# Performance work log

Hardware: AMD Instinct MI355X
Metric: run time of the kernel (lower is better)

## Reference

```python
import jax, jax.numpy as jnp
import numpy as np

NUM_HEADS = 16
LAMBDA = 0.1
HADAMARD_SCALE = 0.05
ROPE_BASE = 10000.0


def _rope(t):
    # t: [B, H, S, hd] -- rotary embedding (half-split convention)
    hd = t.shape[-1]
    S = t.shape[2]
    half = hd // 2
    inv_freq = 1.0 / (ROPE_BASE ** (jnp.arange(half, dtype=jnp.float32) / half))
    ang = jnp.arange(S, dtype=jnp.float32)[:, None] * inv_freq[None, :]  # [S, half]
    cos = jnp.cos(ang).astype(t.dtype)
    sin = jnp.sin(ang).astype(t.dtype)
    t1, t2 = t[..., :half], t[..., half:]
    return jnp.concatenate([t1 * cos - t2 * sin, t2 * cos + t1 * sin], axis=-1)


def _rotate_half(t):
    half = t.shape[-1] // 2
    return jnp.concatenate([-t[..., half:], t[..., :half]], axis=-1)


def setup_inputs() -> dict:
    key = jax.random.key(0)
    ks = jax.random.split(key, 6)
    B, S, D = 2, 2048, 1024
    scale = 1.0 / np.sqrt(D).astype(np.float32)
    x = jax.random.normal(ks[0], (B, S, D), jnp.float32)
    Wq = jax.random.normal(ks[1], (D, D), jnp.float32) * scale
    Wk = jax.random.normal(ks[2], (D, D), jnp.float32) * scale
    Wv = jax.random.normal(ks[3], (D, D), jnp.float32) * scale
    Wo = jax.random.normal(ks[4], (D, D), jnp.float32) * scale
    gate_w = jax.random.normal(ks[5], (D // NUM_HEADS,), jnp.float32) * 0.01
    return {"x": x, "Wq": Wq, "Wk": Wk, "Wv": Wv, "Wo": Wo, "gate_w": gate_w}


def reference(x, Wq, Wk, Wv, Wo, gate_w):
    B, S, D = x.shape
    H = NUM_HEADS
    hd = D // H

    def heads(W):
        return (x @ W.T).reshape(B, S, H, hd).transpose(0, 2, 1, 3)  # [B,H,S,hd]

    Q = _rope(heads(Wq))
    K = _rope(heads(Wk))
    V = heads(Wv)

    causal = jnp.tril(jnp.ones((S, S), dtype=bool))
    inv_sqrt_d = 1.0 / jnp.sqrt(jnp.asarray(hd, x.dtype))

    def attend(q, k):
        # first-order + lambda * second-order (elementwise-squared) scores
        s = (jnp.einsum('bhsd,bhtd->bhst', q, k)
             + LAMBDA * jnp.einsum('bhsd,bhtd->bhst', q * q, k * k)) * inv_sqrt_d
        s = jnp.where(causal, s, jnp.asarray(-1e9, s.dtype))
        a = jax.nn.softmax(s, axis=-1)
        return jnp.einsum('bhst,bhtd->bhsd', a, V)

    out1 = attend(Q, K)                                  # standard pass
    out2 = attend(_rotate_half(Q), _rotate_half(K))      # rotated second pass

    # hadamard gate mix of the two passes
    out = 0.5 * (out1 + out2) + HADAMARD_SCALE * (out1 * out2) * gate_w

    out = out.transpose(0, 2, 1, 3).reshape(B, S, D)
    return out @ Wo.T
```

## Files before the change

kernel.cpp:

```cpp
#include <hip/hip_runtime.h>

typedef unsigned short u16;
typedef __attribute__((ext_vector_type(4))) unsigned short u16x4;
typedef __attribute__((ext_vector_type(8))) unsigned short u16x8;
typedef __attribute__((ext_vector_type(8))) short s16x8;
typedef __attribute__((ext_vector_type(4))) float f32x4;

__device__ __forceinline__ u16 f2bf(float f) {
  unsigned int u = __float_as_uint(f);
  u += 0x7FFFu + ((u >> 16) & 1u);
  return (u16)(u >> 16);
}
__device__ __forceinline__ float bf2f(u16 h) {
  return __uint_as_float(((unsigned int)h) << 16);
}

__device__ __forceinline__ void gload_lds16(const u16* g, u16* l) {
  __builtin_amdgcn_global_load_lds(
      (const __attribute__((address_space(1))) unsigned int*)(g),
      (__attribute__((address_space(3))) unsigned int*)(l), 16, 0, 0);
}

__global__ __launch_bounds__(256) void cvt_all(const float* __restrict__ x,
                                               const float* __restrict__ Wq,
                                               const float* __restrict__ Wk,
                                               const float* __restrict__ Wv,
                                               const float* __restrict__ Wo,
                                               u16* __restrict__ xbf,
                                               u16* __restrict__ wbf,
                                               u16* __restrict__ wobf) {
  int blk = blockIdx.x;
  const float* src;
  u16* dst;
  int i;
  if (blk < 4096) {
    src = x; dst = xbf; i = blk * 256 + threadIdx.x;
  } else {
    int wb = blk - 4096;
    int sel = wb >> 10;
    src = (sel == 0) ? Wq : (sel == 1) ? Wk : (sel == 2) ? Wv : Wo;
    dst = (sel < 3) ? (wbf + (size_t)sel * 1048576) : wobf;
    i = (wb & 1023) * 256 + threadIdx.x;
  }
  float4 v = reinterpret_cast<const float4*>(src)[i];
  u16x4 o;
  o.x = f2bf(v.x); o.y = f2bf(v.y); o.z = f2bf(v.z); o.w = f2bf(v.w);
  reinterpret_cast<u16x4*>(dst)[i] = o;
}

__device__ __forceinline__ void store_out(float* p, float v) { *p = v; }
__device__ __forceinline__ void store_out(u16* p, float v) { *p = f2bf(v); }

template <typename OutT, int WM, int WN>
__global__ __launch_bounds__(256) void gemm_bt(const u16* __restrict__ A,
                                               const u16* __restrict__ Bw,
                                               OutT* __restrict__ C, int N, int K) {
  __shared__ u16 As[2][WM * 1024];
  __shared__ u16 Bs[2][WN * 1024];
  const int tid = threadIdx.x;
  const int lane = tid & 63;
  const int wave = tid >> 6;
  const int wm = wave >> 1, wn = wave & 1;
  const int lh = lane & 15, quad = lane >> 4;
  const int q8 = quad * 8;
  const int m0 = blockIdx.y * (WM * 32), n0 = blockIdx.x * (WN * 32);
  constexpr int NCH = 2 * (WM + WN);
  constexpr int PER = NCH / 4;

  auto stage = [&](int buf, int kt) {
    const int kb = kt * 32;
#pragma unroll
    for (int i = 0; i < PER; ++i) {
      const int c = wave * PER + i;
      if (c < 2 * WM) {
        gload_lds16(A + (size_t)(m0 + c * 16 + lh) * K + kb + q8,
                    &As[buf][c * 512 + lane * 8]);
      } else {
        const int rb = c - 2 * WM;
        gload_lds16(Bw + (size_t)(n0 + rb * 16 + lh) * K + kb + q8,
                    &Bs[buf][rb * 512 + lane * 8]);
      }
    }
  };

  f32x4 acc[WM][WN];
#pragma unroll
  for (int i = 0; i < WM; ++i)
#pragma unroll
    for (int j = 0; j < WN; ++j) { acc[i][j][0] = 0.f; acc[i][j][1] = 0.f; acc[i][j][2] = 0.f; acc[i][j][3] = 0.f; }

  const int nkt = K >> 5;
  stage(0, 0);
  __syncthreads();
  for (int kt = 0; kt < nkt; ++kt) {
    const int p = kt & 1;
    if (kt < nkt - 1) stage(1 - p, kt + 1);
    s16x8 af[WM], bf4[WN];
#pragma unroll
    for (int mb = 0; mb < WM; ++mb)
      af[mb] = *reinterpret_cast<const s16x8*>(&As[p][(wm * WM + mb) * 512 + lane * 8]);
#pragma unroll
    for (int nb = 0; nb < WN; ++nb)
      bf4[nb] = *reinterpret_cast<const s16x8*>(&Bs[p][(wn * WN + nb) * 512 + lane * 8]);
#pragma unroll
    for (int mb = 0; mb < WM; ++mb)
#pragma unroll
      for (int nb = 0; nb < WN; ++nb)
        acc[mb][nb] = __builtin_amdgcn_mfma_f32_16x16x32_bf16(af[mb], bf4[nb], acc[mb][nb], 0, 0, 0);
    __syncthreads();
  }
#pragma unroll
  for (int mb = 0; mb < WM; ++mb)
#pragma unroll
    for (int nb = 0; nb < WN; ++nb) {
      const int col = n0 + wn * (WN * 16) + nb * 16 + lh;
#pragma unroll
      for (int r = 0; r < 4; ++r) {
        const int row = m0 + wm * (WM * 16) + mb * 16 + quad * 4 + r;
        store_out(&C[(size_t)row * N + col], acc[mb][nb][r]);
      }
    }
}

__global__ __launch_bounds__(256) void qkv_gemm(const u16* __restrict__ A,
                                                const u16* __restrict__ Bw,
                                                u16* __restrict__ Vt,
                                                u16* __restrict__ Qs,
                                                u16* __restrict__ Kb,
                                                u16* __restrict__ K2b) {
  __shared__ u16 As[2][4096];
  __shared__ u16 Bs[2][4096];
  const int tid = threadIdx.x;
  const int lane = tid & 63;
  const int wave = tid >> 6;
  const int wm = wave >> 1, wn = wave & 1;
  const int lh = lane & 15, quad = lane >> 4;
  const int q8 = quad * 8;
  const int bx = blockIdx.x;
  const int m0 = blockIdx.y * 128, n0 = bx * 128;
  const int K = 1024;

  auto stage = [&](int buf, int kt) {
    const int kb = kt * 32;
#pragma unroll
    for (int i = 0; i < 4; ++i) {
      const int c = wave * 4 + i;
      if (c < 8) {
        gload_lds16(A + (size_t)(m0 + c * 16 + lh) * K + kb + q8,
                    &As[buf][c * 512 + lane * 8]);
      } else {
        const int rb = c - 8;
        gload_lds16(Bw + (size_t)(n0 + rb * 16 + lh) * K + kb + q8,
                    &Bs[buf][rb * 512 + lane * 8]);
      }
    }
  };

  f32x4 acc[4][4];
#pragma unroll
  for (int i = 0; i < 4; ++i)
#pragma unroll
    for (int j = 0; j < 4; ++j) { acc[i][j][0] = 0.f; acc[i][j][1] = 0.f; acc[i][j][2] = 0.f; acc[i][j][3] = 0.f; }

  stage(0, 0);
  __syncthreads();
  for (int kt = 0; kt < 32; ++kt) {
    const int p = kt & 1;
    if (kt < 31) stage(1 - p, kt + 1);
    s16x8 af[4], bf4[4];
#pragma unroll
    for (int mb = 0; mb < 4; ++mb)
      af[mb] = *reinterpret_cast<const s16x8*>(&As[p][(wm * 4 + mb) * 512 + lane * 8]);
#pragma unroll
    for (int nb = 0; nb < 4; ++nb)
      bf4[nb] = *reinterpret_cast<const s16x8*>(&Bs[p][(wn * 4 + nb) * 512 + lane * 8]);
#pragma unroll
    for (int mb = 0; mb < 4; ++mb)
#pragma unroll
      for (int nb = 0; nb < 4; ++nb)
        acc[mb][nb] = __builtin_amdgcn_mfma_f32_16x16x32_bf16(af[mb], bf4[nb], acc[mb][nb], 0, 0, 0);
    __syncthreads();
  }

  if (bx < 16) {
    const bool isQ = (bx < 8);
#pragma unroll
    for (int nb = 0; nb < 2; ++nb) {
      const int d = nb * 16 + lh;
      const float invf = __expf((float)d * -0.2878231366f);
      const int col = n0 + wn * 64 + nb * 16 + lh;
      const int ch = col & 1023;
      const int h = ch >> 6;
#pragma unroll
      for (int mb = 0; mb < 4; ++mb)
#pragma unroll
        for (int r = 0; r < 4; ++r) {
          const int row = m0 + wm * 64 + mb * 16 + quad * 4 + r;
          const int s = row & 2047, b = row >> 11;
          float ang = (float)s * invf;
          float sv, cv;
          __sincosf(ang, &sv, &cv);
          const float v1 = acc[mb][nb][r], v2 = acc[mb][nb + 2][r];
          const float e0 = v1 * cv - v2 * sv;
          const float e1 = v2 * cv + v1 * sv;
          const size_t ofs = (size_t)((b * 16 + h) * 2048 + s) * 64 + d;
          if (isQ) {
            Qs[ofs]      = f2bf(e0 * 0.125f);
            Qs[ofs + 32] = f2bf(e1 * 0.125f);
          } else {
            Kb[ofs]       = f2bf(e0);
            Kb[ofs + 32]  = f2bf(e1);
            K2b[ofs]      = f2bf(e0 * e0);
            K2b[ofs + 32] = f2bf(e1 * e1);
          }
        }
    }
  } else {
#pragma unroll
    for (int mb = 0; mb < 4; ++mb)
#pragma unroll
      for (int nb = 0; nb < 4; ++nb) {
        const int col = n0 + wn * 64 + nb * 16 + lh;
        const int ch = col & 1023;
        const int h = ch >> 6, d = ch & 63;
        const int row0 = m0 + wm * 64 + mb * 16 + quad * 4;
        const int s0 = row0 & 2047, b = row0 >> 11;
        u16x4 o;
#pragma unroll
        for (int r = 0; r < 4; ++r) o[r] = f2bf(acc[mb][nb][r]);
        *reinterpret_cast<u16x4*>(Vt + (size_t)((b * 16 + h) * 64 + d) * 2048 + s0) = o;
      }
  }
}

__global__ __launch_bounds__(256, 2) void attn_kernel(const u16* __restrict__ Qs,
                                                      const u16* __restrict__ Kb,
                                                      const u16* __restrict__ K2b,
                                                      const u16* __restrict__ Vt,
                                                      const float* __restrict__ gate,
                                                      u16* __restrict__ attn,
                                                      float* __restrict__ Opart,
                                                      float* __restrict__ Lpart,
                                                      float* __restrict__ Opart2,
                                                      float* __restrict__ Lpart2) {
  const int bx = blockIdx.x;
  int qi, kt0, kt1, chunk, which;
  bool split;
  if (bx < 32) {
    qi = 15 - (bx >> 2); chunk = bx & 3; split = true; which = 0;
    const int T = 2 * qi + 2;
    kt0 = (chunk * T) >> 2;
    kt1 = (((chunk + 1) * T) >> 2) - 1;
  } else if (bx < 40) {
    const int t = bx - 32;
    qi = 7 - (t >> 1); chunk = t & 1; split = true; which = 1;
    const int nk = qi + 1; kt0 = chunk * nk; kt1 = kt0 + nk - 1;
  } else {
    qi = 43 - bx; split = false; which = 0; chunk = 0; kt0 = 0; kt1 = 2 * qi + 1;
  }
  const int bh = blockIdx.y;
  const int tid = threadIdx.x, lane = tid & 63, wave = tid >> 6;
  const int lh = lane & 15, quad = lane >> 4;
  const int b = bh >> 4, h = bh & 15;
  __shared__ u16 stageS[2][8192];
  __shared__ u16 Pbuf[4][2][1152];
  const int base = qi * 128 + wave * 32;
  const int q8 = quad * 8;

  auto do_stage = [&](int buf, int kt) {
#pragma unroll
    for (int i = 0; i < 4; ++i) {
      const int c = wave * 4 + i;
      const int t2 = c >> 3, f = c & 7, kk = f >> 2, nb = f & 3;
      const u16* src = (t2 ? K2b : Kb) +
          (size_t)(bh * 2048 + kt * 64 + nb * 16 + lh) * 64 + kk * 32 + q8;
      gload_lds16(src, &stageS[buf][t2 * 4096 + f * 512 + lane * 8]);
    }
  };

  s16x8 qf[2][2], q2f[2][2];
#pragma unroll
  for (int mb = 0; mb < 2; ++mb) {
    const size_t qoff = (size_t)(bh * 2048 + base + mb * 16 + lh) * 64 + q8;
#pragma unroll
    for (int kk = 0; kk < 2; ++kk) {
      qf[mb][kk] = *reinterpret_cast<const s16x8*>(Qs + qoff + kk * 32);
#pragma unroll
      for (int j = 0; j < 8; ++j) {
        float f = bf2f((u16)qf[mb][kk][j]);
        q2f[mb][kk][j] = (short)f2bf(f * f * 0.8f);
      }
    }
  }

  f32x4 oacc[2][4];
  float lsum[2][4];
#pragma unroll
  for (int mb = 0; mb < 2; ++mb)
#pragma unroll
    for (int nb = 0; nb < 4; ++nb) { oacc[mb][nb][0] = 0.f; oacc[mb][nb][1] = 0.f; oacc[mb][nb][2] = 0.f; oacc[mb][nb][3] = 0.f; }
#pragma unroll
  for (int mb = 0; mb < 2; ++mb)
#pragma unroll
    for (int r = 0; r < 4; ++r) lsum[mb][r] = 0.f;
  float gw[4];
#pragma unroll
  for (int nb = 0; nb < 4; ++nb) gw[nb] = gate[nb * 16 + lh];

  do_stage(0, kt0);
  __syncthreads();

  const int wmaxrow = base + 31;
  for (int kt = kt0; kt <= kt1; ++kt) {
    const int p = (kt - kt0) & 1;
    if (kt < kt1) do_stage(1 - p, kt + 1);

    if (kt * 64 <= wmaxrow) {
      const u16* Ks = stageS[p];
      f32x4 sacc[2][4];
#pragma unroll
      for (int mb = 0; mb < 2; ++mb)
#pragma unroll
        for (int nb = 0; nb < 4; ++nb) { sacc[mb][nb][0] = -8.f; sacc[mb][nb][1] = -8.f; sacc[mb][nb][2] = -8.f; sacc[mb][nb][3] = -8.f; }
#pragma unroll
      for (int nb = 0; nb < 4; ++nb)
#pragma unroll
        for (int kk = 0; kk < 2; ++kk) {
          s16x8 kf  = *reinterpret_cast<const s16x8*>(&Ks[(kk * 4 + nb) * 512 + lane * 8]);
          s16x8 k2f = *reinterpret_cast<const s16x8*>(&Ks[4096 + (kk * 4 + nb) * 512 + lane * 8]);
#pragma unroll
          for (int mb = 0; mb < 2; ++mb) {
            sacc[mb][nb] = __builtin_amdgcn_mfma_f32_16x16x32_bf16(qf[mb][kk],  kf,  sacc[mb][nb], 0, 0, 0);
            sacc[mb][nb] = __builtin_amdgcn_mfma_f32_16x16x32_bf16(q2f[mb][kk], k2f, sacc[mb][nb], 0, 0, 0);
          }
        }
      s16x8 vf[2][4];
#pragma unroll
      for (int kk = 0; kk < 2; ++kk)
#pragma unroll
        for (int nb = 0; nb < 4; ++nb)
          vf[kk][nb] = *reinterpret_cast<const s16x8*>(
              Vt + (size_t)(bh * 64 + nb * 16 + lh) * 2048 + kt * 64 + kk * 32 + q8);

      if (kt * 64 + 63 > base) {
#pragma unroll
        for (int mb = 0; mb < 2; ++mb)
#pragma unroll
          for (int nb = 0; nb < 4; ++nb) {
            const int colg = kt * 64 + nb * 16 + lh;
#pragma unroll
            for (int r = 0; r < 4; ++r) {
              const int rowg = base + mb * 16 + quad * 4 + r;
              if (colg > rowg) sacc[mb][nb][r] = -1e9f;
            }
          }
      }
#pragma unroll
      for (int mb = 0; mb < 2; ++mb)
#pragma unroll
        for (int nb = 0; nb < 4; ++nb)
#pragma unroll
          for (int r = 0; r < 4; ++r) {
            float pv = __expf(sacc[mb][nb][r]);
            lsum[mb][r] += pv;
            Pbuf[wave][mb][(quad * 4 + r) * 72 + nb * 16 + lh] = f2bf(pv);
          }
#pragma unroll
      for (int mb = 0; mb < 2; ++mb)
#pragma unroll
        for (int kk = 0; kk < 2; ++kk) {
          s16x8 pf = *reinterpret_cast<const s16x8*>(&Pbuf[wave][mb][lh * 72 + kk * 32 + q8]);
#pragma unroll
          for (int nb = 0; nb < 4; ++nb)
            oacc[mb][nb] = __builtin_amdgcn_mfma_f32_16x16x32_bf16(pf, vf[kk][nb], oacc[mb][nb], 0, 0, 0);
        }
    }
    __syncthreads();
  }
#pragma unroll
  for (int mb = 0; mb < 2; ++mb)
#pragma unroll
    for (int r = 0; r < 4; ++r) {
      float rs = lsum[mb][r];
#pragma unroll
      for (int off = 1; off < 16; off <<= 1) rs += __shfl_xor(rs, off);
      lsum[mb][r] = rs;
    }
  if (split) {
#pragma unroll
    for (int mb = 0; mb < 2; ++mb)
#pragma unroll
      for (int r = 0; r < 4; ++r) {
        const int rowg = base + mb * 16 + quad * 4 + r;
        if (which == 0) {
          const size_t orow = (size_t)chunk * 32768 + bh * 1024 + (rowg - 1024);
          if (lh == 0) Lpart[orow] = lsum[mb][r];
#pragma unroll
          for (int nb = 0; nb < 4; ++nb)
            Opart[orow * 64 + nb * 16 + lh] = oacc[mb][nb][r];
        } else {
          const size_t orow = (size_t)chunk * 16384 + bh * 512 + (rowg - 512);
          if (lh == 0) Lpart2[orow] = lsum[mb][r];
#pragma unroll
          for (int nb = 0; nb < 4; ++nb)
            Opart2[orow * 64 + nb * 16 + lh] = oacc[mb][nb][r];
        }
      }
  } else {
#pragma unroll
    for (int mb = 0; mb < 2; ++mb)
#pragma unroll
      for (int r = 0; r < 4; ++r) {
        const float invl = 1.0f / lsum[mb][r];
        const int rows = base + mb * 16 + quad * 4 + r;
#pragma unroll
        for (int nb = 0; nb < 4; ++nb) {
          float o = oacc[mb][nb][r] * invl;
          float val = o + 0.05f * o * o * gw[nb];
          attn[(size_t)(b * 2048 + rows) * 1024 + h * 64 + nb * 16 + lh] = f2bf(val);
        }
      }
  }
}

__global__ __launch_bounds__(256) void combine_kernel(const float* __restrict__ Opart,
                                                      const float* __restrict__ Lpart,
                                                      const float* __restrict__ Opart2,
                                                      const float* __restrict__ Lpart2,
                                                      const float* __restrict__ gate,
                                                      u16* __restrict__ attn) {
  int idx = blockIdx.x * 256 + threadIdx.x;
  int d = idx & 63;
  int r_all = idx >> 6;
  float o, l;
  int bh, s;
  if (r_all < 32768) {
    o = Opart[idx] + Opart[idx + 2097152] + Opart[idx + 4194304] + Opart[idx + 6291456];
    l = Lpart[r_all] + Lpart[r_all + 32768] + Lpart[r_all + 65536] + Lpart[r_all + 98304];
    bh = r_all >> 10; s = 1024 + (r_all & 1023);
  } else {
    const int r2 = r_all - 32768;
    const int i2 = idx - 2097152;
    o = Opart2[i2] + Opart2[i2 + 1048576];
    l = Lpart2[r2] + Lpart2[r2 + 16384];
    bh = r2 >> 9; s = 512 + (r2 & 511);
  }
  o /= l;
  float val = o + 0.05f * o * o * gate[d];
  int b = bh >> 4, h = bh & 15;
  attn[(size_t)(b * 2048 + s) * 1024 + h * 64 + d] = f2bf(val);
}

extern "C" void kernel_launch(void* const* d_in, const int* in_sizes, int n_in,
                              void* d_out, int out_size, void* d_ws, size_t ws_size,
                              hipStream_t stream) {
  (void)in_sizes; (void)n_in; (void)out_size; (void)ws_size;
  const float* x    = (const float*)d_in[0];
  const float* Wq   = (const float*)d_in[1];
  const float* Wk   = (const float*)d_in[2];
  const float* Wv   = (const float*)d_in[3];
  const float* Wo   = (const float*)d_in[4];
  const float* gate = (const float*)d_in[5];

  u16* ws    = (u16*)d_ws;
  u16* xbf   = ws;
  u16* wbf   = xbf + 4194304;
  u16* wobf  = wbf + 3145728;
  u16* Qsb   = wobf + 1048576;
  u16* Kbb   = Qsb + 4194304;
  u16* K2bb  = Kbb + 4194304;
  u16* Vtb   = K2bb + 4194304;
  float* Opart  = (float*)(Vtb + 4194304);
  float* Lpart  = Opart + 8388608;
  float* Opart2 = Lpart + 131072;
  float* Lpart2 = Opart2 + 2097152;
  u16* attnb = xbf;

  cvt_all<<<8192, 256, 0, stream>>>(x, Wq, Wk, Wv, Wo, xbf, wbf, wobf);
  qkv_gemm<<<dim3(24, 32), 256, 0, stream>>>(xbf, wbf, Vtb, Qsb, Kbb, K2bb);
  attn_kernel<<<dim3(44, 32), 256, 0, stream>>>(Qsb, Kbb, K2bb, Vtb, gate, attnb,
                                                Opart, Lpart, Opart2, Lpart2);
  combine_kernel<<<12288, 256, 0, stream>>>(Opart, Lpart, Opart2, Lpart2, gate, attnb);
  gemm_bt<float, 4, 2><<<dim3(16, 32), 256, 0, stream>>>(attnb, wobf, (float*)d_out, 1024, 1024);
}
```

Baseline: 244.0 us.

## Drop LDS K staging, load K directly, remap blocks per XCD, raise occupancy

Removes the double-buffered shared-memory staging of K and K² tiles and the per-iteration __syncthreads, so each wave reads its K fragments straight from global memory. Each wave stops its loop at its own diagonal tile instead of idling inside a block-wide barrier. Blocks are remapped so the 44 query chunks of a head land on the same XCD for L2 reuse, and launch bounds go from 2 to 4 blocks per CU. s_setprio hints are added around the MFMA sections. The cost is redundant global/L2 traffic for K across the four waves and more register pressure under the higher occupancy bound.

```diff
diff --git a/kernel.cpp b/kernel.cpp
--- a/kernel.cpp
+++ b/kernel.cpp
@@ -233,7 +233,7 @@
   }
 }
 
-__global__ __launch_bounds__(256, 2) void attn_kernel(const u16* __restrict__ Qs,
+__global__ __launch_bounds__(256, 4) void attn_kernel(const u16* __restrict__ Qs,
                                                       const u16* __restrict__ Kb,
                                                       const u16* __restrict__ K2b,
                                                       const u16* __restrict__ Vt,
@@ -243,41 +243,33 @@
                                                       float* __restrict__ Lpart,
                                                       float* __restrict__ Opart2,
                                                       float* __restrict__ Lpart2) {
-  const int bx = blockIdx.x;
+  const int lin = blockIdx.y * 44 + blockIdx.x;
+  const int xcd = lin & 7;
+  const int slot = lin >> 3;
+  const int bh = xcd * 4 + (slot / 44);
+  const int bxv = slot % 44;
+
   int qi, kt0, kt1, chunk, which;
   bool split;
-  if (bx < 32) {
-    qi = 15 - (bx >> 2); chunk = bx & 3; split = true; which = 0;
+  if (bxv < 32) {
+    qi = 15 - (bxv >> 2); chunk = bxv & 3; split = true; which = 0;
     const int T = 2 * qi + 2;
     kt0 = (chunk * T) >> 2;
     kt1 = (((chunk + 1) * T) >> 2) - 1;
-  } else if (bx < 40) {
-    const int t = bx - 32;
+  } else if (bxv < 40) {
+    const int t = bxv - 32;
     qi = 7 - (t >> 1); chunk = t & 1; split = true; which = 1;
     const int nk = qi + 1; kt0 = chunk * nk; kt1 = kt0 + nk - 1;
   } else {
-    qi = 43 - bx; split = false; which = 0; chunk = 0; kt0 = 0; kt1 = 2 * qi + 1;
-  }
-  const int bh = blockIdx.y;
+    qi = 43 - bxv; split = false; which = 0; chunk = 0; kt0 = 0; kt1 = 2 * qi + 1;
+  }
   const int tid = threadIdx.x, lane = tid & 63, wave = tid >> 6;
   const int lh = lane & 15, quad = lane >> 4;
   const int b = bh >> 4, h = bh & 15;
-  __shared__ u16 stageS[2][8192];
   __shared__ u16 Pbuf[4][2][1152];
   const int base = qi * 128 + wave * 32;
   const int q8 = quad * 8;
 
-  auto do_stage = [&](int buf, int kt) {
-#pragma unroll
-    for (int i = 0; i < 4; ++i) {
-      const int c = wave * 4 + i;
-      const int t2 = c >> 3, f = c & 7, kk = f >> 2, nb = f & 3;
-      const u16* src = (t2 ? K2b : Kb) +
-          (size_t)(bh * 2048 + kt * 64 + nb * 16 + lh) * 64 + kk * 32 + q8;
-      gload_lds16(src, &stageS[buf][t2 * 4096 + f * 512 + lane * 8]);
-    }
-  };
-
   s16x8 qf[2][2], q2f[2][2];
 #pragma unroll
   for (int mb = 0; mb < 2; ++mb) {
@@ -307,75 +299,74 @@
 #pragma unroll
   for (int nb = 0; nb < 4; ++nb) gw[nb] = gate[nb * 16 + lh];
 
-  do_stage(0, kt0);
-  __syncthreads();
-
   const int wmaxrow = base + 31;
-  for (int kt = kt0; kt <= kt1; ++kt) {
-    const int p = (kt - kt0) & 1;
-    if (kt < kt1) do_stage(1 - p, kt + 1);
-
-    if (kt * 64 <= wmaxrow) {
-      const u16* Ks = stageS[p];
-      f32x4 sacc[2][4];
+  const int ktdiag = wmaxrow >> 6;
+  const int ktw1 = (kt1 < ktdiag) ? kt1 : ktdiag;
+
+  for (int kt = kt0; kt <= ktw1; ++kt) {
+    f32x4 sacc[2][4];
+#pragma unroll
+    for (int mb = 0; mb < 2; ++mb)
+#pragma unroll
+      for (int nb = 0; nb < 4; ++nb) { sacc[mb][nb][0] = -8.f; sacc[mb][nb][1] = -8.f; sacc[mb][nb][2] = -8.f; sacc[mb][nb][3] = -8.f; }
+    __builtin_amdgcn_s_setprio(1);
+#pragma unroll
+    for (int nb = 0; nb < 4; ++nb) {
+      const size_t krow = (size_t)(bh * 2048 + kt * 64 + nb * 16 + lh) * 64 + q8;
+#pragma unroll
+      for (int kk = 0; kk < 2; ++kk) {
+        s16x8 kf  = *reinterpret_cast<const s16x8*>(Kb  + krow + kk * 32);
+        s16x8 k2f = *reinterpret_cast<const s16x8*>(K2b + krow + kk * 32);
+#pragma unroll
+        for (int mb = 0; mb < 2; ++mb) {
+          sacc[mb][nb] = __builtin_amdgcn_mfma_f32_16x16x32_bf16(qf[mb][kk],  kf,  sacc[mb][nb], 0, 0, 0);
+          sacc[mb][nb] = __builtin_amdgcn_mfma_f32_16x16x32_bf16(q2f[mb][kk], k2f, sacc[mb][nb], 0, 0, 0);
+        }
+      }
+    }
+    __builtin_amdgcn_s_setprio(0);
+    s16x8 vf[2][4];
+#pragma unroll
+    for (int kk = 0; kk < 2; ++kk)
+#pragma unroll
+      for (int nb = 0; nb < 4; ++nb)
+        vf[kk][nb] = *reinterpret_cast<const s16x8*>(
+            Vt + (size_t)(bh * 64 + nb * 16 + lh) * 2048 + kt * 64 + kk * 32 + q8);
+
+    if (kt * 64 + 63 > base) {
 #pragma unroll
       for (int mb = 0; mb < 2; ++mb)
 #pragma unroll
-        for (int nb = 0; nb < 4; ++nb) { sacc[mb][nb][0] = -8.f; sacc[mb][nb][1] = -8.f; sacc[mb][nb][2] = -8.f; sacc[mb][nb][3] = -8.f; }
+        for (int nb = 0; nb < 4; ++nb) {
+          const int colg = kt * 64 + nb * 16 + lh;
+#pragma unroll
+          for (int r = 0; r < 4; ++r) {
+            const int rowg = base + mb * 16 + quad * 4 + r;
+            if (colg > rowg) sacc[mb][nb][r] = -1e9f;
+          }
+        }
+    }
+#pragma unroll
+    for (int mb = 0; mb < 2; ++mb)
 #pragma unroll
       for (int nb = 0; nb < 4; ++nb)
 #pragma unroll
-        for (int kk = 0; kk < 2; ++kk) {
-          s16x8 kf  = *reinterpret_cast<const s16x8*>(&Ks[(kk * 4 + nb) * 512 + lane * 8]);
-          s16x8 k2f = *reinterpret_cast<const s16x8*>(&Ks[4096 + (kk * 4 + nb) * 512 + lane * 8]);
-#pragma unroll
-          for (int mb = 0; mb < 2; ++mb) {
-            sacc[mb][nb] = __builtin_amdgcn_mfma_f32_16x16x32_bf16(qf[mb][kk],  kf,  sacc[mb][nb], 0, 0, 0);
-            sacc[mb][nb] = __builtin_amdgcn_mfma_f32_16x16x32_bf16(q2f[mb][kk], k2f, sacc[mb][nb], 0, 0, 0);
-          }
-        }
-      s16x8 vf[2][4];
-#pragma unroll
-      for (int kk = 0; kk < 2; ++kk)
+        for (int r = 0; r < 4; ++r) {
+          float pv = __expf(sacc[mb][nb][r]);
+          lsum[mb][r] += pv;
+          Pbuf[wave][mb][(quad * 4 + r) * 72 + nb * 16 + lh] = f2bf(pv);
+        }
+    __builtin_amdgcn_s_setprio(1);
+#pragma unroll
+    for (int mb = 0; mb < 2; ++mb)
+#pragma unroll
+      for (int kk = 0; kk < 2; ++kk) {
+        s16x8 pf = *reinterpret_cast<const s16x8*>(&Pbuf[wave][mb][lh * 72 + kk * 32 + q8]);
 #pragma unroll
         for (int nb = 0; nb < 4; ++nb)
-          vf[kk][nb] = *reinterpret_cast<const s16x8*>(
-              Vt + (size_t)(bh * 64 + nb * 16 + lh) * 2048 + kt * 64 + kk * 32 + q8);
-
-      if (kt * 64 + 63 > base) {
-#pragma unroll
-        for (int mb = 0; mb < 2; ++mb)
-#pragma unroll
-          for (int nb = 0; nb < 4; ++nb) {
-            const int colg = kt * 64 + nb * 16 + lh;
-#pragma unroll
-            for (int r = 0; r < 4; ++r) {
-              const int rowg = base + mb * 16 + quad * 4 + r;
-              if (colg > rowg) sacc[mb][nb][r] = -1e9f;
-            }
-          }
-      }
-#pragma unroll
-      for (int mb = 0; mb < 2; ++mb)
-#pragma unroll
-        for (int nb = 0; nb < 4; ++nb)
-#pragma unroll
-          for (int r = 0; r < 4; ++r) {
-            float pv = __expf(sacc[mb][nb][r]);
-            lsum[mb][r] += pv;
-            Pbuf[wave][mb][(quad * 4 + r) * 72 + nb * 16 + lh] = f2bf(pv);
-          }
-#pragma unroll
-      for (int mb = 0; mb < 2; ++mb)
-#pragma unroll
-        for (int kk = 0; kk < 2; ++kk) {
-          s16x8 pf = *reinterpret_cast<const s16x8*>(&Pbuf[wave][mb][lh * 72 + kk * 32 + q8]);
-#pragma unroll
-          for (int nb = 0; nb < 4; ++nb)
-            oacc[mb][nb] = __builtin_amdgcn_mfma_f32_16x16x32_bf16(pf, vf[kk][nb], oacc[mb][nb], 0, 0, 0);
-        }
-    }
-    __syncthreads();
+          oacc[mb][nb] = __builtin_amdgcn_mfma_f32_16x16x32_bf16(pf, vf[kk][nb], oacc[mb][nb], 0, 0, 0);
+      }
+    __builtin_amdgcn_s_setprio(0);
   }
 #pragma unroll
   for (int mb = 0; mb < 2; ++mb)
```

After: 379.2 us. 1.55x slower.

## Prefetch V fragments one tile ahead, remap blocks per XCD, add MFMA priority

Applied to the files above, without the earlier changes.

The attention kernel now loads the V register fragments for the next key tile while the current tile is computed, which hides global-load latency behind the QK and PV MFMAs. Blocks are remapped so that all tiles for a given batch-head land on the same XCD, aiming for better L2 reuse of K and V. s_setprio raises wave priority around the MFMA sections. This costs extra VGPRs for the vnext buffer, which could reduce occupancy under launch_bounds(256,2).

```diff
diff --git a/kernel.cpp b/kernel.cpp
--- a/kernel.cpp
+++ b/kernel.cpp
@@ -243,22 +243,26 @@
                                                       float* __restrict__ Lpart,
                                                       float* __restrict__ Opart2,
                                                       float* __restrict__ Lpart2) {
-  const int bx = blockIdx.x;
+  const int lin = blockIdx.y * 44 + blockIdx.x;
+  const int xcd = lin & 7;
+  const int slot = lin >> 3;
+  const int bh = xcd * 4 + (slot / 44);
+  const int bxv = slot % 44;
+
   int qi, kt0, kt1, chunk, which;
   bool split;
-  if (bx < 32) {
-    qi = 15 - (bx >> 2); chunk = bx & 3; split = true; which = 0;
+  if (bxv < 32) {
+    qi = 15 - (bxv >> 2); chunk = bxv & 3; split = true; which = 0;
     const int T = 2 * qi + 2;
     kt0 = (chunk * T) >> 2;
     kt1 = (((chunk + 1) * T) >> 2) - 1;
-  } else if (bx < 40) {
-    const int t = bx - 32;
+  } else if (bxv < 40) {
+    const int t = bxv - 32;
     qi = 7 - (t >> 1); chunk = t & 1; split = true; which = 1;
     const int nk = qi + 1; kt0 = chunk * nk; kt1 = kt0 + nk - 1;
   } else {
-    qi = 43 - bx; split = false; which = 0; chunk = 0; kt0 = 0; kt1 = 2 * qi + 1;
-  }
-  const int bh = blockIdx.y;
+    qi = 43 - bxv; split = false; which = 0; chunk = 0; kt0 = 0; kt1 = 2 * qi + 1;
+  }
   const int tid = threadIdx.x, lane = tid & 63, wave = tid >> 6;
   const int lh = lane & 15, quad = lane >> 4;
   const int b = bh >> 4, h = bh & 15;
@@ -278,6 +282,15 @@
     }
   };
 
+  auto loadV = [&](s16x8 (&dst)[2][4], int kt) {
+#pragma unroll
+    for (int kk = 0; kk < 2; ++kk)
+#pragma unroll
+      for (int nb = 0; nb < 4; ++nb)
+        dst[kk][nb] = *reinterpret_cast<const s16x8*>(
+            Vt + (size_t)(bh * 64 + nb * 16 + lh) * 2048 + kt * 64 + kk * 32 + q8);
+  };
+
   s16x8 qf[2][2], q2f[2][2];
 #pragma unroll
   for (int mb = 0; mb < 2; ++mb) {
@@ -307,13 +320,19 @@
 #pragma unroll
   for (int nb = 0; nb < 4; ++nb) gw[nb] = gate[nb * 16 + lh];
 
+  s16x8 vf[2][4];
+  loadV(vf, kt0);
   do_stage(0, kt0);
   __syncthreads();
 
   const int wmaxrow = base + 31;
   for (int kt = kt0; kt <= kt1; ++kt) {
     const int p = (kt - kt0) & 1;
-    if (kt < kt1) do_stage(1 - p, kt + 1);
+    if (kt < kt1) {
+      do_stage(1 - p, kt + 1);
+    }
+    s16x8 vnext[2][4];
+    if (kt < kt1) loadV(vnext, kt + 1);
 
     if (kt * 64 <= wmaxrow) {
       const u16* Ks = stageS[p];
@@ -322,6 +341,7 @@
       for (int mb = 0; mb < 2; ++mb)
 #pragma unroll
         for (int nb = 0; nb < 4; ++nb) { sacc[mb][nb][0] = -8.f; sacc[mb][nb][1] = -8.f; sacc[mb][nb][2] = -8.f; sacc[mb][nb][3] = -8.f; }
+      __builtin_amdgcn_s_setprio(1);
 #pragma unroll
       for (int nb = 0; nb < 4; ++nb)
 #pragma unroll
@@ -334,13 +354,7 @@
             sacc[mb][nb] = __builtin_amdgcn_mfma_f32_16x16x32_bf16(q2f[mb][kk], k2f, sacc[mb][nb], 0, 0, 0);
           }
         }
-      s16x8 vf[2][4];
-#pragma unroll
-      for (int kk = 0; kk < 2; ++kk)
-#pragma unroll
-        for (int nb = 0; nb < 4; ++nb)
-          vf[kk][nb] = *reinterpret_cast<const s16x8*>(
-              Vt + (size_t)(bh * 64 + nb * 16 + lh) * 2048 + kt * 64 + kk * 32 + q8);
+      __builtin_amdgcn_s_setprio(0);
 
       if (kt * 64 + 63 > base) {
 #pragma unroll
@@ -365,6 +379,7 @@
             lsum[mb][r] += pv;
             Pbuf[wave][mb][(quad * 4 + r) * 72 + nb * 16 + lh] = f2bf(pv);
           }
+      __builtin_amdgcn_s_setprio(1);
 #pragma unroll
       for (int mb = 0; mb < 2; ++mb)
 #pragma unroll
@@ -374,8 +389,15 @@
           for (int nb = 0; nb < 4; ++nb)
             oacc[mb][nb] = __builtin_amdgcn_mfma_f32_16x16x32_bf16(pf, vf[kk][nb], oacc[mb][nb], 0, 0, 0);
         }
+      __builtin_amdgcn_s_setprio(0);
     }
     __syncthreads();
+    if (kt < kt1) {
+#pragma unroll
+      for (int kk = 0; kk < 2; ++kk)
+#pragma unroll
+        for (int nb = 0; nb < 4; ++nb) vf[kk][nb] = vnext[kk][nb];
+    }
   }
 #pragma unroll
   for (int mb = 0; mb < 2; ++mb)
```

Measured after the change: 244.6 us. Within noise of the previous version (+0.2%).
